# Optimization experiments

Hardware: AMD Instinct MI355X
Metric: run time of the kernel (lower is better)

Reference implementation:

```python
import jax, jax.numpy as jnp
import numpy as np

K = 4
V = 32000
H = 512
B = 16
SOS = 1
EOS = 2


def setup_inputs() -> dict:
    key = jax.random.key(0)
    ks = jax.random.split(key, 8)
    s = 0.08  # small init keeps GRU/log_softmax well-conditioned
    return {
        "enc_h": jax.random.normal(ks[0], (B, H), jnp.float32),
        "E": jax.random.normal(ks[1], (V, H), jnp.float32) * s,
        "W_ih": jax.random.normal(ks[2], (H, 3 * H), jnp.float32) * s,
        "W_hh": jax.random.normal(ks[3], (H, 3 * H), jnp.float32) * s,
        "b_ih": jax.random.normal(ks[4], (3 * H,), jnp.float32) * s,
        "b_hh": jax.random.normal(ks[5], (3 * H,), jnp.float32) * s,
        "Wo": jax.random.normal(ks[6], (H, V), jnp.float32) * s,
        "bo": jax.random.normal(ks[7], (V,), jnp.float32) * s,
        "max_length": 32,
    }


def _beam_search(enc_h, E, W_ih, W_hh, b_ih, b_hh, Wo, bo, T):
    BK = B * K
    pos = jnp.arange(B, dtype=jnp.int32) * K  # pos_index
    # torch .repeat beam inflation: tiled layout (index i -> original i % B)
    h0 = jnp.tile(enc_h, (K, 1))  # [BK, H]
    inp0 = jnp.full((BK,), SOS, dtype=jnp.int32)
    ss0 = jnp.full((BK,), -jnp.inf, dtype=enc_h.dtype).at[pos].set(0.0)

    def gru(x, h):
        gi = x @ W_ih + b_ih
        gh = h @ W_hh + b_hh
        ir, iz, inn = jnp.split(gi, 3, axis=-1)
        hr, hz, hn = jnp.split(gh, 3, axis=-1)
        r = jax.nn.sigmoid(ir + hr)
        z = jax.nn.sigmoid(iz + hz)
        n = jnp.tanh(inn + r * hn)
        return (1.0 - z) * n + z * h

    def fwd_step(carry, _):
        inp, h, ss = carry
        h_new = gru(E[inp], h)                                   # [BK, H]
        logp = jax.nn.log_softmax(h_new @ Wo + bo, axis=-1)      # [BK, V]
        total = (ss[:, None] + logp).reshape(B, K * V)
        scores, cand = jax.lax.top_k(total, K)                   # [B, K]
        symbols = (cand % V).astype(jnp.int32).reshape(-1)       # input_var
        preds = (cand // V + pos[:, None]).astype(jnp.int32).reshape(-1)
        h_sel = h_new[preds]                                     # index_select hidden
        ss_new = scores.reshape(-1)
        ss_masked = jnp.where(symbols == EOS, -jnp.inf, ss_new)  # EOS masking
        return (symbols, h_sel, ss_masked), (logp, ss_new, preds, symbols, h_sel)

    _, (logps, step_scores, preds, syms, hiddens) = jax.lax.scan(
        fwd_step, (inp0, h0, ss0), None, length=T)

    # ---------------- backtrack ----------------
    last = step_scores[-1].reshape(B, K)
    s0, sorted_idx = jax.lax.top_k(last, K)
    tpred0 = (sorted_idx.astype(jnp.int32) + pos[:, None]).reshape(-1)
    lens0 = jnp.full((B, K), T, dtype=jnp.int32)
    hn0 = jnp.zeros((BK, H), dtype=enc_h.dtype)
    eos0 = jnp.zeros((B,), dtype=jnp.int32)

    def bt_step(carry, xs):
        tpred, eosf, s, lens, hn = carry
        logp_t, hid_t, pred_t, sym_t, score_t, tt = xs
        cur_out = logp_t[tpred]
        cur_hid = hid_t[tpred]
        cur_sym = sym_t[tpred]
        new_pred = pred_t[tpred]
        eos = sym_t == EOS
        eos_bk = eos.reshape(B, K).astype(jnp.int32)
        # original loop processes eos hits in descending beam order per batch
        higher = jnp.cumsum(eos_bk[:, ::-1], axis=1)[:, ::-1] - eos_bk
        occ = eosf[:, None] + higher
        res_k = K - occ % K - 1
        res_flat = (pos[:, None] + res_k).reshape(-1)
        idx = jnp.where(eos, res_flat, BK)  # BK = out of bounds -> dropped
        new_pred = new_pred.at[idx].set(pred_t, mode='drop')
        cur_out = cur_out.at[idx].set(logp_t, mode='drop')
        cur_hid = cur_hid.at[idx].set(hid_t, mode='drop')
        hn = hn.at[idx].set(hid_t, mode='drop')
        cur_sym = cur_sym.at[idx].set(sym_t, mode='drop')
        s = s.reshape(-1).at[idx].set(score_t, mode='drop').reshape(B, K)
        lens = lens.reshape(-1).at[idx].set(tt + 1, mode='drop').reshape(B, K)
        eosf = eosf + eos_bk.sum(axis=1)
        return (new_pred, eosf, s, lens, hn), (cur_out, cur_sym)

    ts = jnp.arange(T - 1, -1, -1, dtype=jnp.int32)
    (_, _, s_fin, lens_fin, hn_fin), (outs_rev, syms_rev) = jax.lax.scan(
        bt_step, (tpred0, eos0, s0, lens0, hn0),
        (logps[::-1], hiddens[::-1], preds[::-1], syms[::-1], step_scores[::-1], ts))

    s_sorted, re_idx = jax.lax.top_k(s_fin, K)
    lens_sorted = jnp.take_along_axis(lens_fin, re_idx, axis=1)
    re_flat = (re_idx.astype(jnp.int32) + pos[:, None]).reshape(-1)
    outs = outs_rev[::-1][:, re_flat].reshape(T, B, K, V)
    seqs = syms_rev[::-1][:, re_flat].reshape(T, B, K)
    decoder_outputs = outs[:, :, 0, :]            # [T, B, V]
    decoder_hidden = hn_fin[re_flat].reshape(B, K, H)[:, 0, :]
    return decoder_outputs, decoder_hidden, s_sorted, lens_sorted, seqs


def reference(enc_h, E, W_ih, W_hh, b_ih, b_hh, Wo, bo, max_length):
    return _beam_search(enc_h, E, W_ih, W_hh, b_ih, b_hh, Wo, bo, int(max_length))
```

## Files before the change

kernel.cpp:

```cpp
#include <hip/hip_runtime.h>
#include <math.h>
#include <limits.h>

#define T_STEPS 32
#define BATCH   16
#define KBEAM   4
#define BKR     64
#define HD      512
#define VOC     32000
#define G3      1536
#define SOS_TOK 1
#define EOS_TOK 2
#define NSP     (VOC/64)
#define NE      (NSP*4)
#define NBG     (G3/64)
#define FMBL    2

#define OFF_HCUR   ((size_t)0)
#define OFF_GBUF   (OFF_HCUR + (size_t)BKR*HD)
#define OFF_HNEW   (OFF_GBUF + (size_t)2*BKR*G3)
#define OFF_LSE    (OFF_HNEW + (size_t)T_STEPS*BKR*HD)
#define OFF_SS     (OFF_LSE + (size_t)T_STEPS*BKR)
#define OFF_SCORES (OFF_SS + BKR)
#define OFF_HNFIN  (OFF_SCORES + (size_t)T_STEPS*BKR)
#define OFF_PV     (OFF_HNFIN + (size_t)BKR*HD)
#define OFF_PM     (OFF_PV + (size_t)BKR*NE)
#define OFF_PS     (OFF_PM + (size_t)BKR*NSP)
#define OFF_FEND   (OFF_PS + (size_t)BKR*NSP)
#define IOFF_INP    0
#define IOFF_PREDS  64
#define IOFF_SYMS   (IOFF_PREDS + T_STEPS*BKR)
#define IOFF_RMAP   (IOFF_SYMS + T_STEPS*BKR)
#define IOFF_PC     (IOFF_RMAP + T_STEPS*BATCH)
#define IOFF_GCNT   (IOFF_PC + BKR*NE)
#define IOFF_LCNT   (IOFF_GCNT + T_STEPS)
#define IOFF_END    (IOFF_LCNT + T_STEPS)
#define S_WOH   ((size_t)0)
#define S_WOL   (S_WOH + (size_t)NSP*16*2048)
#define S_WGH   (S_WOL + (size_t)NSP*16*2048)
#define S_WGL   (S_WGH + (size_t)2*NBG*16*2048)
#define S_HNH   (S_WGL + (size_t)2*NBG*16*2048)
#define S_HNL   (S_HNH + (size_t)T_STEPS*BKR*HD)
#define S_HCH   (S_HNL + (size_t)T_STEPS*BKR*HD)
#define S_HCL   (S_HCH + (size_t)BKR*HD)
#define S_EIH   (S_HCL + (size_t)BKR*HD)
#define S_EIL   (S_EIH + (size_t)BKR*HD)
#define S_END   (S_EIL + (size_t)BKR*HD)

#define O_HID  ((size_t)T_STEPS*BATCH*VOC)
#define O_SSRT (O_HID + (size_t)BATCH*HD)
#define O_LENS (O_SSRT + BATCH*KBEAM)
#define O_SEQS (O_LENS + BATCH*KBEAM)

typedef short bf16x8 __attribute__((ext_vector_type(8)));
typedef float f32x4  __attribute__((ext_vector_type(4)));

#define TSZ 2560

__device__ __forceinline__ unsigned short f2bf(float x){
    unsigned u = __float_as_uint(x);
    return (unsigned short)((u + 0x7fffu + ((u >> 16) & 1u)) >> 16);
}
__device__ __forceinline__ float bf2f(unsigned short h){
    return __uint_as_float(((unsigned)h) << 16);
}

__device__ __forceinline__ void dump_C(f32x4 (&acc)[4], float (*Cs)[65], int wave, int lane){
    #pragma unroll
    for (int g = 0; g < 4; ++g){
        int row = g * 16 + (lane >> 4) * 4;
        int col = wave * 16 + (lane & 15);
        #pragma unroll
        for (int r = 0; r < 4; ++r) Cs[row + r][col] = acc[g][r];
    }
}

__device__ __forceinline__ void ins4(float* bv, int* bc, float s, int c){
    bool g0 = (s > bv[0]) || (s == bv[0] && c < bc[0]);
    bool g1 = (s > bv[1]) || (s == bv[1] && c < bc[1]);
    bool g2 = (s > bv[2]) || (s == bv[2] && c < bc[2]);
    bool g3 = (s > bv[3]) || (s == bv[3] && c < bc[3]);
    if (g0){ bv[3]=bv[2];bc[3]=bc[2]; bv[2]=bv[1];bc[2]=bc[1]; bv[1]=bv[0];bc[1]=bc[0]; bv[0]=s; bc[0]=c; }
    else if (g1){ bv[3]=bv[2];bc[3]=bc[2]; bv[2]=bv[1];bc[2]=bc[1]; bv[1]=s; bc[1]=c; }
    else if (g2){ bv[3]=bv[2];bc[3]=bc[2]; bv[2]=s; bc[2]=c; }
    else if (g3){ bv[3]=s; bc[3]=c; }
}


__global__ __launch_bounds__(256) void prepack_kernel(const float* __restrict__ W, int N,
    unsigned short* __restrict__ oh, unsigned short* __restrict__ ol)
{
    const int bx = blockIdx.x, kt = blockIdx.y, tid = threadIdx.x;
    const int bn = tid >> 2, kq = (tid & 3) * 8;
    union { unsigned short u[8]; uint4 v; } h8, l8;
    #pragma unroll
    for (int j = 0; j < 8; ++j){
        float x = W[(size_t)(kt*32 + kq + j) * (size_t)N + bx*64 + bn];
        unsigned short h = f2bf(x);
        h8.u[j] = h; l8.u[j] = f2bf(x - bf2f(h));
    }
    const size_t base = ((size_t)bx*16 + kt) * 2048 + (size_t)tid * 8;
    *(uint4*)(oh + base) = h8.v;
    *(uint4*)(ol + base) = l8.v;
}

__global__ __launch_bounds__(256) void gates_pre_kernel(
    const unsigned short* __restrict__ eih, const unsigned short* __restrict__ eil,
    const unsigned short* __restrict__ hch, const unsigned short* __restrict__ hcl,
    const unsigned short* __restrict__ wgh, const unsigned short* __restrict__ wgl,
    const float* __restrict__ b_ih, const float* __restrict__ b_hh,
    float* __restrict__ gbuf,
    const float* __restrict__ h_cur, float* __restrict__ h_new,
    unsigned short* __restrict__ hnh, unsigned short* __restrict__ hnl,
    int* __restrict__ gcnt)
{
    __shared__ __align__(16) unsigned short sm[2*4*TSZ];
    const int z = blockIdx.y, bx = blockIdx.x, n0 = bx * 64;
    const int tid = threadIdx.x;
    const unsigned short* ahg = z ? hch : eih;
    const unsigned short* alg = z ? hcl : eil;
    const size_t bt = ((size_t)z*NBG + bx) * 16 * 2048;
    const unsigned short* bth = wgh + bt;
    const unsigned short* btl = wgl + bt;
    const int row = tid >> 2, kq = (tid & 3) * 8;
    const int wave = tid >> 6, lane = tid & 63;
    const int fr = lane & 15, fq = lane >> 4;
    const int wr = row * 40 + kq;
    f32x4 acc[4];
    #pragma unroll
    for (int g = 0; g < 4; ++g) acc[g] = (f32x4){0.f,0.f,0.f,0.f};
    {
        uint4 a_h = *(const uint4*)(ahg + (size_t)row*512 + kq);
        uint4 a_l = *(const uint4*)(alg + (size_t)row*512 + kq);
        uint4 b_h = *(const uint4*)(bth + (size_t)tid*8);
        uint4 b_l = *(const uint4*)(btl + (size_t)tid*8);
        *(uint4*)(sm + 0*TSZ + wr) = a_h;
        *(uint4*)(sm + 1*TSZ + wr) = a_l;
        *(uint4*)(sm + 2*TSZ + wr) = b_h;
        *(uint4*)(sm + 3*TSZ + wr) = b_l;
    }
    uint4 pa_h = *(const uint4*)(ahg + (size_t)row*512 + 32 + kq);
    uint4 pa_l = *(const uint4*)(alg + (size_t)row*512 + 32 + kq);
    uint4 pb_h = *(const uint4*)(bth + 2048 + (size_t)tid*8);
    uint4 pb_l = *(const uint4*)(btl + 2048 + (size_t)tid*8);
    __syncthreads();
    #pragma unroll 2
    for (int kt = 0; kt < 16; ++kt){
        unsigned short* cb = sm + (kt & 1) * (4*TSZ);
        unsigned short* nbuf = sm + ((kt & 1) ^ 1) * (4*TSZ);
        uint4 na_h = pa_h, na_l = pa_l, nb_h = pb_h, nb_l = pb_l;
        if (kt < 14){
            na_h = *(const uint4*)(ahg + (size_t)row*512 + (kt+2)*32 + kq);
            na_l = *(const uint4*)(alg + (size_t)row*512 + (kt+2)*32 + kq);
            nb_h = *(const uint4*)(bth + (size_t)(kt+2)*2048 + (size_t)tid*8);
            nb_l = *(const uint4*)(btl + (size_t)(kt+2)*2048 + (size_t)tid*8);
        }
        bf16x8 bh = *(const bf16x8*)(cb + 2*TSZ + (wave*16 + fr)*40 + fq*8);
        bf16x8 bl = *(const bf16x8*)(cb + 3*TSZ + (wave*16 + fr)*40 + fq*8);
        #pragma unroll
        for (int g = 0; g < 4; ++g){
            bf16x8 ah = *(const bf16x8*)(cb + 0*TSZ + (g*16 + fr)*40 + fq*8);
            bf16x8 al = *(const bf16x8*)(cb + 1*TSZ + (g*16 + fr)*40 + fq*8);
            acc[g] = __builtin_amdgcn_mfma_f32_16x16x32_bf16(ah, bh, acc[g], 0, 0, 0);
            acc[g] = __builtin_amdgcn_mfma_f32_16x16x32_bf16(ah, bl, acc[g], 0, 0, 0);
            acc[g] = __builtin_amdgcn_mfma_f32_16x16x32_bf16(al, bh, acc[g], 0, 0, 0);
        }
        if (kt < 15){
            *(uint4*)(nbuf + 0*TSZ + wr) = pa_h;
            *(uint4*)(nbuf + 1*TSZ + wr) = pa_l;
            *(uint4*)(nbuf + 2*TSZ + wr) = pb_h;
            *(uint4*)(nbuf + 3*TSZ + wr) = pb_l;
        }
        __syncthreads();
        pa_h = na_h; pa_l = na_l; pb_h = nb_h; pb_l = nb_l;
    }
    const float* bias = z ? b_hh : b_ih;
    const int col = wave*16 + fr;
    const float bz = bias[n0 + col];
    float* gp = gbuf + (size_t)z * BKR * G3 + n0 + col;
    #pragma unroll
    for (int g = 0; g < 4; ++g){
        const int r0 = g*16 + fq*4;
        #pragma unroll
        for (int r = 0; r < 4; ++r)
            gp[(size_t)(r0 + r) * G3] = acc[g][r] + bz;
    }
    __syncthreads();
    int* comm = (int*)sm;
    if (tid == 0){
        __threadfence();
        comm[0] = atomicAdd(gcnt, 1);
    }
    __syncthreads();
    const int old = comm[0];
    if (old >= 2*NBG - 8 && old < 2*NBG){
        if (tid == 0){
            while (__hip_atomic_load(gcnt, __ATOMIC_ACQUIRE, __HIP_MEMORY_SCOPE_AGENT) < 2*NBG)
                __builtin_amdgcn_s_sleep(1);
        }
        __syncthreads();
        __threadfence();
        const int slice = old - (2*NBG - 8);
        for (int x = tid; x < 64*64; x += 256){
            const int rr = x >> 6, j = (slice << 6) + (x & 63);
            const int xi = rr * HD + j;
            const float* gi = gbuf + (size_t)rr * G3;
            const float* gh = gbuf + (size_t)BKR * G3 + (size_t)rr * G3;
            float ir = gi[j], iz = gi[j + 512], inn = gi[j + 1024];
            float hr = gh[j], hz = gh[j + 512], hnv = gh[j + 1024];
            float r  = 1.f / (1.f + expf(-(ir + hr)));
            float zz = 1.f / (1.f + expf(-(iz + hz)));
            float n  = tanhf(inn + r * hnv);
            float v = (1.f - zz) * n + zz * h_cur[xi];
            h_new[xi] = v;
            unsigned short h = f2bf(v);
            hnh[xi] = h; hnl[xi] = f2bf(v - bf2f(h));
        }
    }
}

__global__ __launch_bounds__(256) void logits_pre_kernel(
    const unsigned short* __restrict__ hnh, const unsigned short* __restrict__ hnl,
    const unsigned short* __restrict__ woh, const unsigned short* __restrict__ wol,
    const float* __restrict__ bo,
    float* __restrict__ pv, int* __restrict__ pc, float* __restrict__ pm, float* __restrict__ ps)
{
    __shared__ __align__(16) unsigned short sm[2*4*TSZ];
    const int bx = blockIdx.x, n0 = bx * 64;
    const int tid = threadIdx.x;
    const unsigned short* bth = woh + (size_t)bx * 16 * 2048;
    const unsigned short* btl = wol + (size_t)bx * 16 * 2048;
    const int row = tid >> 2, kq = (tid & 3) * 8;
    const int wave = tid >> 6, lane = tid & 63;
    const int fr = lane & 15, fq = lane >> 4;
    const int wr = row * 40 + kq;
    f32x4 acc[4];
    #pragma unroll
    for (int g = 0; g < 4; ++g) acc[g] = (f32x4){0.f,0.f,0.f,0.f};
    {
        uint4 a_h = *(const uint4*)(hnh + (size_t)row*512 + kq);
        uint4 a_l = *(const uint4*)(hnl + (size_t)row*512 + kq);
        uint4 b_h = *(const uint4*)(bth + (size_t)tid*8);
        uint4 b_l = *(const uint4*)(btl + (size_t)tid*8);
        *(uint4*)(sm + 0*TSZ + wr) = a_h;
        *(uint4*)(sm + 1*TSZ + wr) = a_l;
        *(uint4*)(sm + 2*TSZ + wr) = b_h;
        *(uint4*)(sm + 3*TSZ + wr) = b_l;
    }
    uint4 pa_h = *(const uint4*)(hnh + (size_t)row*512 + 32 + kq);
    uint4 pa_l = *(const uint4*)(hnl + (size_t)row*512 + 32 + kq);
    uint4 pb_h = *(const uint4*)(bth + 2048 + (size_t)tid*8);
    uint4 pb_l = *(const uint4*)(btl + 2048 + (size_t)tid*8);
    __syncthreads();
    #pragma unroll 2
    for (int kt = 0; kt < 16; ++kt){
        unsigned short* cb = sm + (kt & 1) * (4*TSZ);
        unsigned short* nbuf = sm + ((kt & 1) ^ 1) * (4*TSZ);
        uint4 na_h = pa_h, na_l = pa_l, nb_h = pb_h, nb_l = pb_l;
        if (kt < 14){
            na_h = *(const uint4*)(hnh + (size_t)row*512 + (kt+2)*32 + kq);
            na_l = *(const uint4*)(hnl + (size_t)row*512 + (kt+2)*32 + kq);
            nb_h = *(const uint4*)(bth + (size_t)(kt+2)*2048 + (size_t)tid*8);
            nb_l = *(const uint4*)(btl + (size_t)(kt+2)*2048 + (size_t)tid*8);
        }
        bf16x8 bh = *(const bf16x8*)(cb + 2*TSZ + (wave*16 + fr)*40 + fq*8);
        bf16x8 bl = *(const bf16x8*)(cb + 3*TSZ + (wave*16 + fr)*40 + fq*8);
        #pragma unroll
        for (int g = 0; g < 4; ++g){
            bf16x8 ah = *(const bf16x8*)(cb + 0*TSZ + (g*16 + fr)*40 + fq*8);
            bf16x8 al = *(const bf16x8*)(cb + 1*TSZ + (g*16 + fr)*40 + fq*8);
            acc[g] = __builtin_amdgcn_mfma_f32_16x16x32_bf16(ah, bh, acc[g], 0, 0, 0);
            acc[g] = __builtin_amdgcn_mfma_f32_16x16x32_bf16(ah, bl, acc[g], 0, 0, 0);
            acc[g] = __builtin_amdgcn_mfma_f32_16x16x32_bf16(al, bh, acc[g], 0, 0, 0);
        }
        if (kt < 15){
            *(uint4*)(nbuf + 0*TSZ + wr) = pa_h;
            *(uint4*)(nbuf + 1*TSZ + wr) = pa_l;
            *(uint4*)(nbuf + 2*TSZ + wr) = pb_h;
            *(uint4*)(nbuf + 3*TSZ + wr) = pb_l;
        }
        __syncthreads();
        pa_h = na_h; pa_l = na_l; pb_h = nb_h; pb_l = nb_l;
    }
    float (*Cs)[65] = (float(*)[65])sm;
    dump_C(acc, Cs, wave, lane);
    __syncthreads();
    const int c0 = (tid & 3) * 16;
    float bv[4] = {-INFINITY,-INFINITY,-INFINITY,-INFINITY};
    int bc[4] = {INT_MAX, INT_MAX, INT_MAX, INT_MAX};
    float m = -INFINITY, s = 0.f;
    #pragma unroll
    for (int j = 0; j < 16; ++j){
        float x = Cs[row][c0 + j] + bo[n0 + c0 + j];
        if (x > m){ s = s * expf(m - x) + 1.f; m = x; }
        else s += expf(x - m);
        ins4(bv, bc, x, n0 + c0 + j);
    }
    #pragma unroll
    for (int o = 1; o < 4; o <<= 1){
        float ov[4]; int oc[4];
        #pragma unroll
        for (int q = 0; q < 4; ++q){ ov[q] = __shfl_xor(bv[q], o); oc[q] = __shfl_xor(bc[q], o); }
        #pragma unroll
        for (int q = 0; q < 4; ++q) ins4(bv, bc, ov[q], oc[q]);
        float m2 = __shfl_xor(m, o), s2 = __shfl_xor(s, o);
        float M = fmaxf(m, m2);
        s = s * expf(m - M) + s2 * expf(m2 - M);
        m = M;
    }
    if ((tid & 3) == 0){
        const size_t base = (size_t)row * NE + (size_t)bx * 4;
        #pragma unroll
        for (int q = 0; q < 4; ++q){ pv[base + q] = bv[q]; pc[base + q] = bc[q]; }
        pm[row * NSP + bx] = m; ps[row * NSP + bx] = s;
    }
}

__global__ __launch_bounds__(256) void final_pre_kernel(
    const unsigned short* __restrict__ hnh, const unsigned short* __restrict__ hnl,
    const int* __restrict__ rmap, const float* __restrict__ lse_all,
    const unsigned short* __restrict__ woh, const unsigned short* __restrict__ wol,
    const float* __restrict__ bo, float* __restrict__ out)
{
    __shared__ __align__(16) unsigned short sm[2*6*TSZ];
    __shared__ int sidx[64*FMBL]; __shared__ float subm[64*FMBL];
    const int tid = threadIdx.x;
    const int bx = blockIdx.y, n0 = bx * 64;
    const int mbase = blockIdx.x * (64 * FMBL);
    if (tid < 64*FMBL){ int g = rmap[mbase + tid]; sidx[tid] = g; subm[tid] = lse_all[g]; }
    __syncthreads();
    const int row = tid >> 2, kq = (tid & 3) * 8;
    const int wave = tid >> 6, lane = tid & 63;
    const int fr = lane & 15, fq = lane >> 4;
    const int wr = row * 40 + kq;
    const size_t r0 = (size_t)sidx[row] * 512;
    const size_t r1 = (size_t)sidx[64 + row] * 512;
    const unsigned short* bth = woh + (size_t)bx * 16 * 2048;
    const unsigned short* btl = wol + (size_t)bx * 16 * 2048;
    f32x4 acc[FMBL][4];
    #pragma unroll
    for (int mb = 0; mb < FMBL; ++mb)
        #pragma unroll
        for (int g = 0; g < 4; ++g) acc[mb][g] = (f32x4){0.f,0.f,0.f,0.f};
    {
        uint4 a0h = *(const uint4*)(hnh + r0 + kq);
        uint4 a0l = *(const uint4*)(hnl + r0 + kq);
        uint4 a1h = *(const uint4*)(hnh + r1 + kq);
        uint4 a1l = *(const uint4*)(hnl + r1 + kq);
        uint4 b_h = *(const uint4*)(bth + (size_t)tid*8);
        uint4 b_l = *(const uint4*)(btl + (size_t)tid*8);
        *(uint4*)(sm + 0*TSZ + wr) = a0h;
        *(uint4*)(sm + 1*TSZ + wr) = a0l;
        *(uint4*)(sm + 2*TSZ + wr) = a1h;
        *(uint4*)(sm + 3*TSZ + wr) = a1l;
        *(uint4*)(sm + 4*TSZ + wr) = b_h;
        *(uint4*)(sm + 5*TSZ + wr) = b_l;
    }
    uint4 p0h = *(const uint4*)(hnh + r0 + 32 + kq);
    uint4 p0l = *(const uint4*)(hnl + r0 + 32 + kq);
    uint4 p1h = *(const uint4*)(hnh + r1 + 32 + kq);
    uint4 p1l = *(const uint4*)(hnl + r1 + 32 + kq);
    uint4 pbh = *(const uint4*)(bth + 2048 + (size_t)tid*8);
    uint4 pbl = *(const uint4*)(btl + 2048 + (size_t)tid*8);
    __syncthreads();
    #pragma unroll 2
    for (int kt = 0; kt < 16; ++kt){
        unsigned short* cb = sm + (kt & 1) * (6*TSZ);
        unsigned short* nbuf = sm + ((kt & 1) ^ 1) * (6*TSZ);
        uint4 n0h = p0h, n0l = p0l, n1h = p1h, n1l = p1l, nbh = pbh, nbl = pbl;
        if (kt < 14){
            n0h = *(const uint4*)(hnh + r0 + (kt+2)*32 + kq);
            n0l = *(const uint4*)(hnl + r0 + (kt+2)*32 + kq);
            n1h = *(const uint4*)(hnh + r1 + (kt+2)*32 + kq);
            n1l = *(const uint4*)(hnl + r1 + (kt+2)*32 + kq);
            nbh = *(const uint4*)(bth + (size_t)(kt+2)*2048 + (size_t)tid*8);
            nbl = *(const uint4*)(btl + (size_t)(kt+2)*2048 + (size_t)tid*8);
        }
        bf16x8 bh = *(const bf16x8*)(cb + 4*TSZ + (wave*16 + fr)*40 + fq*8);
        bf16x8 bl = *(const bf16x8*)(cb + 5*TSZ + (wave*16 + fr)*40 + fq*8);
        #pragma unroll
        for (int mb = 0; mb < FMBL; ++mb){
            #pragma unroll
            for (int g = 0; g < 4; ++g){
                bf16x8 ah = *(const bf16x8*)(cb + (2*mb+0)*TSZ + (g*16 + fr)*40 + fq*8);
                bf16x8 al = *(const bf16x8*)(cb + (2*mb+1)*TSZ + (g*16 + fr)*40 + fq*8);
                acc[mb][g] = __builtin_amdgcn_mfma_f32_16x16x32_bf16(ah, bh, acc[mb][g], 0, 0, 0);
                acc[mb][g] = __builtin_amdgcn_mfma_f32_16x16x32_bf16(ah, bl, acc[mb][g], 0, 0, 0);
                acc[mb][g] = __builtin_amdgcn_mfma_f32_16x16x32_bf16(al, bh, acc[mb][g], 0, 0, 0);
            }
        }
        if (kt < 15){
            *(uint4*)(nbuf + 0*TSZ + wr) = p0h;
            *(uint4*)(nbuf + 1*TSZ + wr) = p0l;
            *(uint4*)(nbuf + 2*TSZ + wr) = p1h;
            *(uint4*)(nbuf + 3*TSZ + wr) = p1l;
            *(uint4*)(nbuf + 4*TSZ + wr) = pbh;
            *(uint4*)(nbuf + 5*TSZ + wr) = pbl;
        }
        __syncthreads();
        p0h = n0h; p0l = n0l; p1h = n1h; p1l = n1l; pbh = nbh; pbl = nbl;
    }
    const int col = n0 + wave*16 + fr;
    const float bz = bo[col];
    #pragma unroll
    for (int mb = 0; mb < FMBL; ++mb){
        #pragma unroll
        for (int g = 0; g < 4; ++g){
            const int rb = mb*64 + g*16 + fq*4;
            #pragma unroll
            for (int r = 0; r < 4; ++r){
                const int rowi = rb + r;
                out[(size_t)(mbase + rowi) * VOC + col] = acc[mb][g][r] + bz - subm[rowi];
            }
        }
    }
}

__device__ __forceinline__ void mfma_core(
    const float* __restrict__ Abase, const int* __restrict__ ridx, int mbase,
    const float* __restrict__ B, int ldb, int n0,
    unsigned short (&Ah)[64][40], unsigned short (&Al)[64][40],
    unsigned short (&Bh)[64][40], unsigned short (&Bl)[64][40],
    int (&sidx)[64], f32x4 (&acc)[4])
{
    const int tid = threadIdx.x;
    if (tid < 64) sidx[tid] = ridx ? ridx[mbase + tid] : (mbase + tid);
    #pragma unroll
    for (int g = 0; g < 4; ++g) acc[g] = (f32x4){0.f, 0.f, 0.f, 0.f};
    const int wave = tid >> 6, lane = tid & 63;
    const int am = tid >> 2, ak0 = (tid & 3) * 8;
    const int bn = tid & 63, br0 = (tid >> 6) * 8;
    __syncthreads();
    const float* bcol = B + n0 + bn;
    for (int kt = 0; kt < 16; ++kt){
        {
            const float* ap = Abase + (size_t)sidx[am] * HD + kt * 32 + ak0;
            float4 x0 = *(const float4*)ap, x1 = *(const float4*)(ap + 4);
            float xs[8] = {x0.x, x0.y, x0.z, x0.w, x1.x, x1.y, x1.z, x1.w};
            union { unsigned short u[8]; uint4 v; } h8, l8;
            #pragma unroll
            for (int j = 0; j < 8; ++j){
                unsigned short h = f2bf(xs[j]);
                h8.u[j] = h; l8.u[j] = f2bf(xs[j] - bf2f(h));
            }
            *(uint4*)&Ah[am][ak0] = h8.v;
            *(uint4*)&Al[am][ak0] = l8.v;
        }
        {
            const float* bp = bcol + (size_t)(kt * 32 + br0) * ldb;
            union { unsigned short u[8]; uint4 v; } h8, l8;
            #pragma unroll
            for (int j = 0; j < 8; ++j){
                float x = bp[(size_t)j * ldb];
                unsigned short h = f2bf(x);
                h8.u[j] = h; l8.u[j] = f2bf(x - bf2f(h));
            }
            *(uint4*)&Bh[bn][br0] = h8.v;
            *(uint4*)&Bl[bn][br0] = l8.v;
        }
        __syncthreads();
        bf16x8 bh = *(const bf16x8*)&Bh[wave * 16 + (lane & 15)][(lane >> 4) * 8];
        bf16x8 bl = *(const bf16x8*)&Bl[wave * 16 + (lane & 15)][(lane >> 4) * 8];
        #pragma unroll
        for (int g = 0; g < 4; ++g){
            bf16x8 ah = *(const bf16x8*)&Ah[g * 16 + (lane & 15)][(lane >> 4) * 8];
            bf16x8 al = *(const bf16x8*)&Al[g * 16 + (lane & 15)][(lane >> 4) * 8];
            acc[g] = __builtin_amdgcn_mfma_f32_16x16x32_bf16(ah, bh, acc[g], 0, 0, 0);
            acc[g] = __builtin_amdgcn_mfma_f32_16x16x32_bf16(ah, bl, acc[g], 0, 0, 0);
            acc[g] = __builtin_amdgcn_mfma_f32_16x16x32_bf16(al, bh, acc[g], 0, 0, 0);
        }
        __syncthreads();
    }
}

__global__ __launch_bounds__(256) void gates_mfma_kernel(
    const float* __restrict__ E, const int* __restrict__ inp, const float* __restrict__ h_cur,
    const float* __restrict__ W_ih, const float* __restrict__ W_hh,
    const float* __restrict__ b_ih, const float* __restrict__ b_hh,
    float* __restrict__ gbuf)
{
    __shared__ unsigned short Ah[64][40], Al[64][40], Bh[64][40], Bl[64][40];
    __shared__ int sidx[64];
    __shared__ float Cs[64][65];
    const int z = blockIdx.y;
    const int n0 = blockIdx.x * 64;
    const int tid = threadIdx.x;
    f32x4 acc[4];
    mfma_core(z ? h_cur : E, z ? nullptr : inp, 0,
              z ? W_hh : W_ih, G3, n0, Ah, Al, Bh, Bl, sidx, acc);
    dump_C(acc, Cs, tid >> 6, tid & 63);
    __syncthreads();
    const float* bias = z ? b_hh : b_ih;
    const int row = tid >> 2, c0 = (tid & 3) * 16;
    float* gp = gbuf + (size_t)z * BKR * G3 + (size_t)row * G3 + n0 + c0;
    #pragma unroll
    for (int q = 0; q < 4; ++q){
        float4 bz = *(const float4*)(bias + n0 + c0 + q * 4);
        float4 v;
        v.x = Cs[row][c0 + q*4 + 0] + bz.x;
        v.y = Cs[row][c0 + q*4 + 1] + bz.y;
        v.z = Cs[row][c0 + q*4 + 2] + bz.z;
        v.w = Cs[row][c0 + q*4 + 3] + bz.w;
        *(float4*)(gp + q * 4) = v;
    }
}

__global__ __launch_bounds__(256) void logits_topk_kernel(const float* __restrict__ h_new,
    const float* __restrict__ Wo, const float* __restrict__ bo,
    float* __restrict__ pv, int* __restrict__ pc, float* __restrict__ pm, float* __restrict__ ps)
{
    __shared__ unsigned short Ah[64][40], Al[64][40], Bh[64][40], Bl[64][40];
    __shared__ int sidx[64];
    __shared__ float Cs[64][65];
    const int bx = blockIdx.x, n0 = bx * 64;
    const int tid = threadIdx.x;
    f32x4 acc[4];
    mfma_core(h_new, nullptr, 0, Wo, VOC, n0, Ah, Al, Bh, Bl, sidx, acc);
    dump_C(acc, Cs, tid >> 6, tid & 63);
    __syncthreads();
    const int row = tid >> 2, c0 = (tid & 3) * 16;
    float bv[4] = {-INFINITY,-INFINITY,-INFINITY,-INFINITY};
    int bc[4] = {INT_MAX, INT_MAX, INT_MAX, INT_MAX};
    float m = -INFINITY, s = 0.f;
    #pragma unroll
    for (int j = 0; j < 16; ++j){
        float x = Cs[row][c0 + j] + bo[n0 + c0 + j];
        if (x > m){ s = s * expf(m - x) + 1.f; m = x; }
        else s += expf(x - m);
        ins4(bv, bc, x, n0 + c0 + j);
    }
    #pragma unroll
    for (int o = 1; o < 4; o <<= 1){
        float ov[4]; int oc[4];
        #pragma unroll
        for (int q = 0; q < 4; ++q){ ov[q] = __shfl_xor(bv[q], o); oc[q] = __shfl_xor(bc[q], o); }
        #pragma unroll
        for (int q = 0; q < 4; ++q) ins4(bv, bc, ov[q], oc[q]);
        float m2 = __shfl_xor(m, o), s2 = __shfl_xor(s, o);
        float M = fmaxf(m, m2);
        s = s * expf(m - M) + s2 * expf(m2 - M);
        m = M;
    }
    if ((tid & 3) == 0){
        const size_t base = (size_t)row * NE + (size_t)bx * 4;
        #pragma unroll
        for (int q = 0; q < 4; ++q){ pv[base + q] = bv[q]; pc[base + q] = bc[q]; }
        pm[row * NSP + bx] = m; ps[row * NSP + bx] = s;
    }
}

__global__ __launch_bounds__(256) void final_mfma_kernel(const float* __restrict__ h_new_all,
    const int* __restrict__ rmap, const float* __restrict__ lse_all,
    const float* __restrict__ Wo, const float* __restrict__ bo, float* __restrict__ out)
{
    __shared__ unsigned short Ah[64][40], Al[64][40], Bh[64][40], Bl[64][40];
    __shared__ int sidx[64];
    __shared__ float Cs[64][65];
    __shared__ float subm[64];
    const int n0 = blockIdx.x * 64, mb = blockIdx.y * 64;
    const int tid = threadIdx.x;
    f32x4 acc[4];
    mfma_core(h_new_all, rmap, mb, Wo, VOC, n0, Ah, Al, Bh, Bl, sidx, acc);
    dump_C(acc, Cs, tid >> 6, tid & 63);
    if (tid < 64) subm[tid] = lse_all[sidx[tid]];
    __syncthreads();
    const int row = tid >> 2, c0 = (tid & 3) * 16;
    const float sub = subm[row];
    float* op = out + (size_t)(mb + row) * VOC + n0 + c0;
    #pragma unroll
    for (int q = 0; q < 4; ++q){
        float4 bz = *(const float4*)(bo + n0 + c0 + q * 4);
        float4 v;
        v.x = Cs[row][c0 + q*4 + 0] + bz.x - sub;
        v.y = Cs[row][c0 + q*4 + 1] + bz.y - sub;
        v.z = Cs[row][c0 + q*4 + 2] + bz.z - sub;
        v.w = Cs[row][c0 + q*4 + 3] + bz.w - sub;
        *(float4*)(op + q * 4) = v;
    }
}


__global__ void gru_combine_kernel(const float* __restrict__ gbuf, const float* __restrict__ h_cur,
    float* __restrict__ h_new, unsigned short* __restrict__ hnh, unsigned short* __restrict__ hnl)
{
    int x = blockIdx.x * 256 + threadIdx.x;
    int i = x >> 9, j = x & 511;
    const float* gi = gbuf + (size_t)i * G3;
    const float* gh = gbuf + (size_t)BKR * G3 + (size_t)i * G3;
    float ir = gi[j], iz = gi[j + 512], inn = gi[j + 1024];
    float hr = gh[j], hz = gh[j + 512], hnv = gh[j + 1024];
    float r  = 1.f / (1.f + expf(-(ir + hr)));
    float zz = 1.f / (1.f + expf(-(iz + hz)));
    float n  = tanhf(inn + r * hnv);
    float v = (1.f - zz) * n + zz * h_cur[x];
    h_new[x] = v;
    if (hnh){
        unsigned short h = f2bf(v);
        hnh[x] = h; hnl[x] = f2bf(v - bf2f(h));
    }
}

__global__ __launch_bounds__(256) void topk_phase_b(
    const float* __restrict__ pv, const int* __restrict__ pc,
    const float* __restrict__ pm, const float* __restrict__ ps,
    int t,
    float* __restrict__ scores_all, int* __restrict__ preds_all, int* __restrict__ syms_all,
    float* __restrict__ ss, int* __restrict__ inp, float* __restrict__ lse_all,
    const float* __restrict__ h_new, float* __restrict__ h_cur,
    const float* __restrict__ E,
    unsigned short* __restrict__ hch, unsigned short* __restrict__ hcl,
    unsigned short* __restrict__ eih, unsigned short* __restrict__ eil)
{
    const int b = blockIdx.x, tid = threadIdx.x;
    const int wave = tid >> 6, lane = tid & 63;
    const int row = b * KBEAM + wave;

    float bv[4] = {-INFINITY,-INFINITY,-INFINITY,-INFINITY};
    int bc[4] = {INT_MAX, INT_MAX, INT_MAX, INT_MAX};
    for (int e = lane; e < NE; e += 64)
        ins4(bv, bc, pv[(size_t)row * NE + e], pc[(size_t)row * NE + e]);
    #pragma unroll
    for (int o = 1; o < 64; o <<= 1){
        float ov[4]; int oc[4];
        #pragma unroll
        for (int q = 0; q < 4; ++q){ ov[q] = __shfl_xor(bv[q], o); oc[q] = __shfl_xor(bc[q], o); }
        #pragma unroll
        for (int q = 0; q < 4; ++q) ins4(bv, bc, ov[q], oc[q]);
    }
    float m = -INFINITY, s = 0.f;
    for (int e = lane; e < NSP; e += 64){
        float m2 = pm[row * NSP + e], s2 = ps[row * NSP + e];
        float M = fmaxf(m, m2);
        s = s * expf(m - M) + s2 * expf(m2 - M);
        m = M;
    }
    #pragma unroll
    for (int o = 1; o < 64; o <<= 1){
        float m2 = __shfl_xor(m, o), s2 = __shfl_xor(s, o);
        float M = fmaxf(m, m2);
        s = s * expf(m - M) + s2 * expf(m2 - M);
        m = M;
    }
    __shared__ float rtv[KBEAM][4]; __shared__ int rtc[KBEAM][4];
    __shared__ float rlse[KBEAM];
    if (lane == 0){
        #pragma unroll
        for (int q = 0; q < 4; ++q){ rtv[wave][q] = bv[q]; rtc[wave][q] = bc[q]; }
        rlse[wave] = m + logf(s);
    }
    __syncthreads();
    __shared__ int spred[KBEAM]; __shared__ int ssym[KBEAM];
    if (tid == 0){
        float gv[4] = {-INFINITY,-INFINITY,-INFINITY,-INFINITY};
        int gc[4] = {INT_MAX, INT_MAX, INT_MAX, INT_MAX};
        #pragma unroll
        for (int kl = 0; kl < KBEAM; ++kl){
            const int r2 = b * KBEAM + kl;
            float lse = rlse[kl];
            lse_all[t * BKR + r2] = lse;
            float off = ss[r2] - lse;
            if (off == -INFINITY){
                #pragma unroll
                for (int q = 0; q < 4; ++q) ins4(gv, gc, -INFINITY, kl * VOC + q);
            } else {
                #pragma unroll
                for (int q = 0; q < 4; ++q) ins4(gv, gc, rtv[kl][q] + off, kl * VOC + rtc[kl][q]);
            }
        }
        #pragma unroll
        for (int u = 0; u < KBEAM; ++u){
            int cand = gc[u]; float val = gv[u];
            int sym = cand % VOC; int pg = b * KBEAM + cand / VOC;
            int slot = b * KBEAM + u;
            scores_all[t * BKR + slot] = val;
            syms_all[t * BKR + slot] = sym;
            preds_all[t * BKR + slot] = pg;
            ss[slot] = (sym == EOS_TOK) ? -INFINITY : val;
            inp[slot] = sym;
            spred[u] = pg; ssym[u] = sym;
        }
    }
    __syncthreads();
    for (int x = tid; x < KBEAM * HD; x += 256){
        int u = x >> 9, j = x & 511;
        const int idx = (b * KBEAM + u) * HD + j;
        float v = h_new[spred[u] * HD + j];
        h_cur[idx] = v;
        if (hch){
            unsigned short h = f2bf(v);
            hch[idx] = h; hcl[idx] = f2bf(v - bf2f(h));
            float e = E[(size_t)ssym[u] * HD + j];
            unsigned short eh = f2bf(e);
            eih[idx] = eh; eil[idx] = f2bf(e - bf2f(eh));
        }
    }
}

__global__ void init_kernel(const float* __restrict__ enc_h, const float* __restrict__ E,
    float* __restrict__ h_cur, float* __restrict__ ss, int* __restrict__ inp,
    unsigned short* __restrict__ hch, unsigned short* __restrict__ hcl,
    unsigned short* __restrict__ eih, unsigned short* __restrict__ eil,
    int* __restrict__ cnts)
{
    const int i = blockIdx.x;
    for (int j = threadIdx.x; j < HD; j += blockDim.x){
        float v = enc_h[(i & (BATCH - 1)) * HD + j];
        h_cur[i * HD + j] = v;
        if (hch){
            const int idx = i * HD + j;
            unsigned short h = f2bf(v);
            hch[idx] = h; hcl[idx] = f2bf(v - bf2f(h));
            float e = E[(size_t)SOS_TOK * HD + j];
            unsigned short eh = f2bf(e);
            eih[idx] = eh; eil[idx] = f2bf(e - bf2f(eh));
        }
    }
    if (i == 0 && threadIdx.x < BKR){
        ss[threadIdx.x] = ((threadIdx.x & (KBEAM - 1)) == 0) ? 0.f : -INFINITY;
        inp[threadIdx.x] = SOS_TOK;
    }
    if (i == 1 && cnts){
        for (int x = threadIdx.x; x < 2*T_STEPS; x += blockDim.x) cnts[x] = 0;
    }
}

__global__ __launch_bounds__(256) void backtrack_kernel(
    const float* __restrict__ scores_all, const int* __restrict__ preds_all, const int* __restrict__ syms_all,
    const float* __restrict__ h_new_all, float* __restrict__ hn_fin,
    int* __restrict__ rmap, float* __restrict__ out)
{
    __shared__ int   l_syms[T_STEPS*BKR];
    __shared__ int   l_preds[T_STEPS*BKR];
    __shared__ float l_scores[T_STEPS*BKR];
    __shared__ int   outrow_s[T_STEPS*BKR];
    __shared__ int   cursym_s[T_STEPS*BKR];
    __shared__ int tpred[64]; __shared__ float sfin[64]; __shared__ int lensq[64];
    __shared__ int eosf[BATCH];
    __shared__ int orow[64], csym[64], npred_s[64];
    __shared__ int cp_slot[64], cp_src[64]; __shared__ int nc_b[BATCH];
    __shared__ int reidx[64];
    const int tid = threadIdx.x;

    for (int x = tid; x < T_STEPS*BKR; x += 256){
        l_syms[x]   = syms_all[x];
        l_preds[x]  = preds_all[x];
        l_scores[x] = scores_all[x];
    }
    for (int x = tid; x < BKR*HD; x += 256) hn_fin[x] = 0.f;
    __syncthreads();

    if (tid < BATCH){
        const int b = tid;
        float v[KBEAM]; int used[KBEAM];
        #pragma unroll
        for (int k = 0; k < KBEAM; ++k){ v[k] = l_scores[(T_STEPS-1)*BKR + b*KBEAM + k]; used[k] = 0; }
        #pragma unroll
        for (int u = 0; u < KBEAM; ++u){
            int best = -1; float bvv = 0.f;
            #pragma unroll
            for (int k = 0; k < KBEAM; ++k) if (!used[k] && (best < 0 || v[k] > bvv)){ best = k; bvv = v[k]; }
            used[best] = 1;
            tpred[b*KBEAM+u] = b*KBEAM + best;
            sfin[b*KBEAM+u] = bvv;
            lensq[b*KBEAM+u] = T_STEPS;
        }
        eosf[b] = 0;
    }
    __syncthreads();

    for (int t = T_STEPS-1; t >= 0; --t){
        if (tid < 64){
            int tp = tpred[tid];
            orow[tid]    = tp;
            csym[tid]    = l_syms[t*BKR + tp];
            npred_s[tid] = l_preds[t*BKR + tp];
        }
        __syncthreads();
        if (tid < BATCH){
            const int b = tid;
            int eos[KBEAM]; int cnt = 0;
            #pragma unroll
            for (int k = 0; k < KBEAM; ++k) eos[k] = (l_syms[t*BKR + b*KBEAM + k] == EOS_TOK);
            int nc = 0;
            #pragma unroll
            for (int k = 0; k < KBEAM; ++k) if (eos[k]){
                int higher = 0;
                #pragma unroll
                for (int k2 = k+1; k2 < KBEAM; ++k2) higher += eos[k2];
                int occ = eosf[b] + higher;
                int rk = KBEAM - (occ % KBEAM) - 1;
                int slot = b*KBEAM + rk;
                int j = b*KBEAM + k;
                npred_s[slot] = l_preds[t*BKR + j];
                orow[slot]    = j;
                csym[slot]    = l_syms[t*BKR + j];
                sfin[slot]    = l_scores[t*BKR + j];
                lensq[slot]   = t + 1;
                cp_slot[b*KBEAM + nc] = slot;
                cp_src[b*KBEAM + nc]  = l_preds[t*BKR + j];
                ++nc; ++cnt;
            }
            nc_b[b] = nc;
            eosf[b] += cnt;
        }
        __syncthreads();
        if (tid < 64){
            outrow_s[t*BKR + tid] = orow[tid];
            cursym_s[t*BKR + tid] = csym[tid];
            tpred[tid] = npred_s[tid];
        }
        {
            const int e = tid >> 2;
            const int eb = e >> 2, eq = e & 3;
            if (eq < nc_b[eb]){
                const int slot = cp_slot[eb*KBEAM + eq];
                const int src  = cp_src[eb*KBEAM + eq];
                const float4* sp = (const float4*)(h_new_all + (size_t)(t*BKR + src)*HD);
                float4* dp = (float4*)(hn_fin + (size_t)slot*HD);
                for (int j = (tid & 3); j < HD/4; j += 4) dp[j] = sp[j];
            }
        }
        __syncthreads();
    }

    if (tid < BATCH){
        const int b = tid;
        float v[KBEAM]; int used[KBEAM];
        #pragma unroll
        for (int k = 0; k < KBEAM; ++k){ v[k] = sfin[b*KBEAM+k]; used[k] = 0; }
        #pragma unroll
        for (int u = 0; u < KBEAM; ++u){
            int best = -1; float bvv = 0.f;
            #pragma unroll
            for (int k = 0; k < KBEAM; ++k) if (!used[k] && (best < 0 || v[k] > bvv)){ best = k; bvv = v[k]; }
            used[best] = 1;
            reidx[b*KBEAM+u] = best;
            out[O_SSRT + b*KBEAM + u] = bvv;
            out[O_LENS + b*KBEAM + u] = (float)lensq[b*KBEAM + best];
        }
    }
    __syncthreads();
    for (int x = tid; x < T_STEPS*BATCH; x += 256){
        int t2 = x >> 4, b = x & 15;
        rmap[x] = t2*BKR + outrow_s[t2*BKR + b*KBEAM + reidx[b*KBEAM]];
    }
    for (int x = tid; x < T_STEPS*BKR; x += 256){
        int t2 = x >> 6, rem = x & 63, b = rem >> 2, k = rem & 3;
        out[O_SEQS + x] = (float)cursym_s[t2*BKR + b*KBEAM + reidx[b*KBEAM + k]];
    }
    for (int x = tid; x < BATCH*HD; x += 256){
        int b = x >> 9, j = x & 511;
        out[O_HID + x] = hn_fin[(b*KBEAM + reidx[b*KBEAM])*HD + j];
    }
}

extern "C" void kernel_launch(void* const* d_in, const int* in_sizes, int n_in,
                              void* d_out, int out_size, void* d_ws, size_t ws_size,
                              hipStream_t stream)
{
    const float* enc_h = (const float*)d_in[0];
    const float* E     = (const float*)d_in[1];
    const float* W_ih  = (const float*)d_in[2];
    const float* W_hh  = (const float*)d_in[3];
    const float* b_ih  = (const float*)d_in[4];
    const float* b_hh  = (const float*)d_in[5];
    const float* Wo    = (const float*)d_in[6];
    const float* bo    = (const float*)d_in[7];
    float* out = (float*)d_out;

    float* w = (float*)d_ws;
    float* h_cur      = w + OFF_HCUR;
    float* gbuf       = w + OFF_GBUF;
    float* h_new_all  = w + OFF_HNEW;
    float* lse_all    = w + OFF_LSE;
    float* ss         = w + OFF_SS;
    float* scores_all = w + OFF_SCORES;
    float* hn_fin     = w + OFF_HNFIN;
    float* pv         = w + OFF_PV;
    float* pm         = w + OFF_PM;
    float* ps         = w + OFF_PS;
    int* wi         = (int*)(w + OFF_FEND);
    int* inp        = wi + IOFF_INP;
    int* preds_all  = wi + IOFF_PREDS;
    int* syms_all   = wi + IOFF_SYMS;
    int* rmap       = wi + IOFF_RMAP;
    int* pc         = wi + IOFF_PC;
    int* gcnt       = wi + IOFF_GCNT;
    unsigned short* sb = (unsigned short*)(wi + IOFF_END);
    unsigned short* woh = sb + S_WOH;
    unsigned short* wol = sb + S_WOL;
    unsigned short* wgh = sb + S_WGH;
    unsigned short* wgl = sb + S_WGL;
    unsigned short* hnh = sb + S_HNH;
    unsigned short* hnl = sb + S_HNL;
    unsigned short* hch = sb + S_HCH;
    unsigned short* hcl = sb + S_HCL;
    unsigned short* eih = sb + S_EIH;
    unsigned short* eil = sb + S_EIL;

    const size_t NEED = (size_t)OFF_FEND*4 + (size_t)IOFF_END*4 + (size_t)S_END*2;
    const bool pre = (ws_size >= NEED);

    init_kernel<<<dim3(BKR), 256, 0, stream>>>(enc_h, E, h_cur, ss, inp,
        pre ? hch : nullptr, hcl, eih, eil, pre ? gcnt : nullptr);
    if (pre){
        prepack_kernel<<<dim3(NSP, 16), 256, 0, stream>>>(Wo, VOC, woh, wol);
        prepack_kernel<<<dim3(NBG, 16), 256, 0, stream>>>(W_ih, G3, wgh, wgl);
        prepack_kernel<<<dim3(NBG, 16), 256, 0, stream>>>(W_hh, G3,
            wgh + (size_t)NBG*16*2048, wgl + (size_t)NBG*16*2048);
    }
    for (int t = 0; t < T_STEPS; ++t){
        float* h_new_t = h_new_all + (size_t)t * BKR * HD;
        unsigned short* hnh_t = hnh + (size_t)t * BKR * HD;
        unsigned short* hnl_t = hnl + (size_t)t * BKR * HD;
        if (pre){
            gates_pre_kernel<<<dim3(NBG, 2), 256, 0, stream>>>(eih, eil, hch, hcl,
                wgh, wgl, b_ih, b_hh, gbuf, h_cur, h_new_t, hnh_t, hnl_t, gcnt + t);
            logits_pre_kernel<<<dim3(NSP), 256, 0, stream>>>(hnh_t, hnl_t, woh, wol, bo,
                pv, pc, pm, ps);
            topk_phase_b<<<dim3(BATCH), 256, 0, stream>>>(pv, pc, pm, ps, t, scores_all, preds_all, syms_all,
                ss, inp, lse_all, h_new_t, h_cur, E,
                hch, hcl, eih, eil);
        } else {
            gates_mfma_kernel<<<dim3(NBG, 2), 256, 0, stream>>>(E, inp, h_cur, W_ih, W_hh, b_ih, b_hh, gbuf);
            gru_combine_kernel<<<dim3(BKR*HD/256), 256, 0, stream>>>(gbuf, h_cur, h_new_t,
                nullptr, hnl_t);
            logits_topk_kernel<<<dim3(NSP), 256, 0, stream>>>(h_new_t, Wo, bo, pv, pc, pm, ps);
            topk_phase_b<<<dim3(BATCH), 256, 0, stream>>>(pv, pc, pm, ps, t, scores_all, preds_all, syms_all,
                ss, inp, lse_all, h_new_t, h_cur, E,
                nullptr, hcl, eih, eil);
        }
    }
    backtrack_kernel<<<dim3(1), 256, 0, stream>>>(scores_all, preds_all, syms_all, h_new_all, hn_fin,
                                                  rmap, out);
    if (pre){
        final_pre_kernel<<<dim3((T_STEPS*BATCH)/(64*FMBL), NSP), 256, 0, stream>>>(
            hnh, hnl, rmap, lse_all, woh, wol, bo, out);
    } else {
        final_mfma_kernel<<<dim3(NSP, T_STEPS*BATCH/64), 256, 0, stream>>>(h_new_all, rmap, lse_all, Wo, bo, out);
    }
}
```

Measured before the change: 3.023 ms.

## Drop LDS staging in MFMA GEMM kernels and load fragments directly from global

Removes the double-buffered shared-memory staging of A and B tiles in the gates, logits and final-output GEMM kernels. Each wave now loads its MFMA fragments straight from global memory, with the A fragments of the gathered-row kernel taken through precomputed row indices. This drops the LDS writes, the per-k-tile barriers and the LDS footprint, which may allow more blocks per CU. In exchange, A fragments are loaded redundantly by all four waves and the loads are less coalesced, relying on L1/L2 to absorb the duplication, and there is no explicit prefetch pipelining.

After: 4.277 ms. +41.5%, slower.

```diff
diff --git a/kernel.cpp b/kernel.cpp
--- a/kernel.cpp
+++ b/kernel.cpp
@@ -55,8 +55,6 @@
 typedef short bf16x8 __attribute__((ext_vector_type(8)));
 typedef float f32x4  __attribute__((ext_vector_type(4)));
 
-#define TSZ 2560
-
 __device__ __forceinline__ unsigned short f2bf(float x){
     unsigned u = __float_as_uint(x);
     return (unsigned short)((u + 0x7fffu + ((u >> 16) & 1u)) >> 16);
@@ -114,65 +112,33 @@
     unsigned short* __restrict__ hnh, unsigned short* __restrict__ hnl,
     int* __restrict__ gcnt)
 {
-    __shared__ __align__(16) unsigned short sm[2*4*TSZ];
+    __shared__ int comm[1];
     const int z = blockIdx.y, bx = blockIdx.x, n0 = bx * 64;
     const int tid = threadIdx.x;
     const unsigned short* ahg = z ? hch : eih;
     const unsigned short* alg = z ? hcl : eil;
     const size_t bt = ((size_t)z*NBG + bx) * 16 * 2048;
-    const unsigned short* bth = wgh + bt;
-    const unsigned short* btl = wgl + bt;
-    const int row = tid >> 2, kq = (tid & 3) * 8;
     const int wave = tid >> 6, lane = tid & 63;
     const int fr = lane & 15, fq = lane >> 4;
-    const int wr = row * 40 + kq;
+    const unsigned short* bh_p = wgh + bt + (wave*16 + fr)*32 + fq*8;
+    const unsigned short* bl_p = wgl + bt + (wave*16 + fr)*32 + fq*8;
+    const unsigned short* ah_p = ahg + (size_t)fr*512 + fq*8;
+    const unsigned short* al_p = alg + (size_t)fr*512 + fq*8;
     f32x4 acc[4];
     #pragma unroll
     for (int g = 0; g < 4; ++g) acc[g] = (f32x4){0.f,0.f,0.f,0.f};
-    {
-        uint4 a_h = *(const uint4*)(ahg + (size_t)row*512 + kq);
-        uint4 a_l = *(const uint4*)(alg + (size_t)row*512 + kq);
-        uint4 b_h = *(const uint4*)(bth + (size_t)tid*8);
-        uint4 b_l = *(const uint4*)(btl + (size_t)tid*8);
-        *(uint4*)(sm + 0*TSZ + wr) = a_h;
-        *(uint4*)(sm + 1*TSZ + wr) = a_l;
-        *(uint4*)(sm + 2*TSZ + wr) = b_h;
-        *(uint4*)(sm + 3*TSZ + wr) = b_l;
-    }
-    uint4 pa_h = *(const uint4*)(ahg + (size_t)row*512 + 32 + kq);
-    uint4 pa_l = *(const uint4*)(alg + (size_t)row*512 + 32 + kq);
-    uint4 pb_h = *(const uint4*)(bth + 2048 + (size_t)tid*8);
-    uint4 pb_l = *(const uint4*)(btl + 2048 + (size_t)tid*8);
-    __syncthreads();
-    #pragma unroll 2
+    #pragma unroll 4
     for (int kt = 0; kt < 16; ++kt){
-        unsigned short* cb = sm + (kt & 1) * (4*TSZ);
-        unsigned short* nbuf = sm + ((kt & 1) ^ 1) * (4*TSZ);
-        uint4 na_h = pa_h, na_l = pa_l, nb_h = pb_h, nb_l = pb_l;
-        if (kt < 14){
-            na_h = *(const uint4*)(ahg + (size_t)row*512 + (kt+2)*32 + kq);
-            na_l = *(const uint4*)(alg + (size_t)row*512 + (kt+2)*32 + kq);
-            nb_h = *(const uint4*)(bth + (size_t)(kt+2)*2048 + (size_t)tid*8);
-            nb_l = *(const uint4*)(btl + (size_t)(kt+2)*2048 + (size_t)tid*8);
-        }
-        bf16x8 bh = *(const bf16x8*)(cb + 2*TSZ + (wave*16 + fr)*40 + fq*8);
-        bf16x8 bl = *(const bf16x8*)(cb + 3*TSZ + (wave*16 + fr)*40 + fq*8);
+        bf16x8 bh = *(const bf16x8*)(bh_p + kt*2048);
+        bf16x8 bl = *(const bf16x8*)(bl_p + kt*2048);
         #pragma unroll
         for (int g = 0; g < 4; ++g){
-            bf16x8 ah = *(const bf16x8*)(cb + 0*TSZ + (g*16 + fr)*40 + fq*8);
-            bf16x8 al = *(const bf16x8*)(cb + 1*TSZ + (g*16 + fr)*40 + fq*8);
+            bf16x8 ah = *(const bf16x8*)(ah_p + g*16*512 + kt*32);
+            bf16x8 al = *(const bf16x8*)(al_p + g*16*512 + kt*32);
             acc[g] = __builtin_amdgcn_mfma_f32_16x16x32_bf16(ah, bh, acc[g], 0, 0, 0);
             acc[g] = __builtin_amdgcn_mfma_f32_16x16x32_bf16(ah, bl, acc[g], 0, 0, 0);
             acc[g] = __builtin_amdgcn_mfma_f32_16x16x32_bf16(al, bh, acc[g], 0, 0, 0);
         }
-        if (kt < 15){
-            *(uint4*)(nbuf + 0*TSZ + wr) = pa_h;
-            *(uint4*)(nbuf + 1*TSZ + wr) = pa_l;
-            *(uint4*)(nbuf + 2*TSZ + wr) = pb_h;
-            *(uint4*)(nbuf + 3*TSZ + wr) = pb_l;
-        }
-        __syncthreads();
-        pa_h = na_h; pa_l = na_l; pb_h = nb_h; pb_l = nb_l;
     }
     const float* bias = z ? b_hh : b_ih;
     const int col = wave*16 + fr;
@@ -186,7 +152,6 @@
             gp[(size_t)(r0 + r) * G3] = acc[g][r] + bz;
     }
     __syncthreads();
-    int* comm = (int*)sm;
     if (tid == 0){
         __threadfence();
         comm[0] = atomicAdd(gcnt, 1);
@@ -225,67 +190,34 @@
     const float* __restrict__ bo,
     float* __restrict__ pv, int* __restrict__ pc, float* __restrict__ pm, float* __restrict__ ps)
 {
-    __shared__ __align__(16) unsigned short sm[2*4*TSZ];
+    __shared__ float Cs[64][65];
     const int bx = blockIdx.x, n0 = bx * 64;
     const int tid = threadIdx.x;
-    const unsigned short* bth = woh + (size_t)bx * 16 * 2048;
-    const unsigned short* btl = wol + (size_t)bx * 16 * 2048;
-    const int row = tid >> 2, kq = (tid & 3) * 8;
     const int wave = tid >> 6, lane = tid & 63;
     const int fr = lane & 15, fq = lane >> 4;
-    const int wr = row * 40 + kq;
+    const unsigned short* bh_p = woh + (size_t)bx*16*2048 + (wave*16 + fr)*32 + fq*8;
+    const unsigned short* bl_p = wol + (size_t)bx*16*2048 + (wave*16 + fr)*32 + fq*8;
+    const unsigned short* ah_p = hnh + (size_t)fr*512 + fq*8;
+    const unsigned short* al_p = hnl + (size_t)fr*512 + fq*8;
     f32x4 acc[4];
     #pragma unroll
     for (int g = 0; g < 4; ++g) acc[g] = (f32x4){0.f,0.f,0.f,0.f};
-    {
-        uint4 a_h = *(const uint4*)(hnh + (size_t)row*512 + kq);
-        uint4 a_l = *(const uint4*)(hnl + (size_t)row*512 + kq);
-        uint4 b_h = *(const uint4*)(bth + (size_t)tid*8);
-        uint4 b_l = *(const uint4*)(btl + (size_t)tid*8);
-        *(uint4*)(sm + 0*TSZ + wr) = a_h;
-        *(uint4*)(sm + 1*TSZ + wr) = a_l;
-        *(uint4*)(sm + 2*TSZ + wr) = b_h;
-        *(uint4*)(sm + 3*TSZ + wr) = b_l;
-    }
-    uint4 pa_h = *(const uint4*)(hnh + (size_t)row*512 + 32 + kq);
-    uint4 pa_l = *(const uint4*)(hnl + (size_t)row*512 + 32 + kq);
-    uint4 pb_h = *(const uint4*)(bth + 2048 + (size_t)tid*8);
-    uint4 pb_l = *(const uint4*)(btl + 2048 + (size_t)tid*8);
-    __syncthreads();
-    #pragma unroll 2
+    #pragma unroll 4
     for (int kt = 0; kt < 16; ++kt){
-        unsigned short* cb = sm + (kt & 1) * (4*TSZ);
-        unsigned short* nbuf = sm + ((kt & 1) ^ 1) * (4*TSZ);
-        uint4 na_h = pa_h, na_l = pa_l, nb_h = pb_h, nb_l = pb_l;
-        if (kt < 14){
-            na_h = *(const uint4*)(hnh + (size_t)row*512 + (kt+2)*32 + kq);
-            na_l = *(const uint4*)(hnl + (size_t)row*512 + (kt+2)*32 + kq);
-            nb_h = *(const uint4*)(bth + (size_t)(kt+2)*2048 + (size_t)tid*8);
-            nb_l = *(const uint4*)(btl + (size_t)(kt+2)*2048 + (size_t)tid*8);
-        }
-        bf16x8 bh = *(const bf16x8*)(cb + 2*TSZ + (wave*16 + fr)*40 + fq*8);
-        bf16x8 bl = *(const bf16x8*)(cb + 3*TSZ + (wave*16 + fr)*40 + fq*8);
+        bf16x8 bh = *(const bf16x8*)(bh_p + kt*2048);
+        bf16x8 bl = *(const bf16x8*)(bl_p + kt*2048);
         #pragma unroll
         for (int g = 0; g < 4; ++g){
-            bf16x8 ah = *(const bf16x8*)(cb + 0*TSZ + (g*16 + fr)*40 + fq*8);
-            bf16x8 al = *(const bf16x8*)(cb + 1*TSZ + (g*16 + fr)*40 + fq*8);
+            bf16x8 ah = *(const bf16x8*)(ah_p + g*16*512 + kt*32);
+            bf16x8 al = *(const bf16x8*)(al_p + g*16*512 + kt*32);
             acc[g] = __builtin_amdgcn_mfma_f32_16x16x32_bf16(ah, bh, acc[g], 0, 0, 0);
             acc[g] = __builtin_amdgcn_mfma_f32_16x16x32_bf16(ah, bl, acc[g], 0, 0, 0);
             acc[g] = __builtin_amdgcn_mfma_f32_16x16x32_bf16(al, bh, acc[g], 0, 0, 0);
         }
-        if (kt < 15){
-            *(uint4*)(nbuf + 0*TSZ + wr) = pa_h;
-            *(uint4*)(nbuf + 1*TSZ + wr) = pa_l;
-            *(uint4*)(nbuf + 2*TSZ + wr) = pb_h;
-            *(uint4*)(nbuf + 3*TSZ + wr) = pb_l;
-        }
-        __syncthreads();
-        pa_h = na_h; pa_l = na_l; pb_h = nb_h; pb_l = nb_l;
-    }
-    float (*Cs)[65] = (float(*)[65])sm;
+    }
     dump_C(acc, Cs, wave, lane);
     __syncthreads();
-    const int c0 = (tid & 3) * 16;
+    const int row = tid >> 2, c0 = (tid & 3) * 16;
     float bv[4] = {-INFINITY,-INFINITY,-INFINITY,-INFINITY};
     int bc[4] = {INT_MAX, INT_MAX, INT_MAX, INT_MAX};
     float m = -INFINITY, s = 0.f;
@@ -322,83 +254,42 @@
     const unsigned short* __restrict__ woh, const unsigned short* __restrict__ wol,
     const float* __restrict__ bo, float* __restrict__ out)
 {
-    __shared__ __align__(16) unsigned short sm[2*6*TSZ];
     __shared__ int sidx[64*FMBL]; __shared__ float subm[64*FMBL];
     const int tid = threadIdx.x;
     const int bx = blockIdx.y, n0 = bx * 64;
     const int mbase = blockIdx.x * (64 * FMBL);
     if (tid < 64*FMBL){ int g = rmap[mbase + tid]; sidx[tid] = g; subm[tid] = lse_all[g]; }
     __syncthreads();
-    const int row = tid >> 2, kq = (tid & 3) * 8;
     const int wave = tid >> 6, lane = tid & 63;
     const int fr = lane & 15, fq = lane >> 4;
-    const int wr = row * 40 + kq;
-    const size_t r0 = (size_t)sidx[row] * 512;
-    const size_t r1 = (size_t)sidx[64 + row] * 512;
-    const unsigned short* bth = woh + (size_t)bx * 16 * 2048;
-    const unsigned short* btl = wol + (size_t)bx * 16 * 2048;
+    int rows[FMBL*4];
+    #pragma unroll
+    for (int mb = 0; mb < FMBL; ++mb)
+        #pragma unroll
+        for (int g = 0; g < 4; ++g) rows[mb*4 + g] = sidx[mb*64 + g*16 + fr];
+    const unsigned short* bh_p = woh + (size_t)bx*16*2048 + (wave*16 + fr)*32 + fq*8;
+    const unsigned short* bl_p = wol + (size_t)bx*16*2048 + (wave*16 + fr)*32 + fq*8;
     f32x4 acc[FMBL][4];
     #pragma unroll
     for (int mb = 0; mb < FMBL; ++mb)
         #pragma unroll
         for (int g = 0; g < 4; ++g) acc[mb][g] = (f32x4){0.f,0.f,0.f,0.f};
-    {
-        uint4 a0h = *(const uint4*)(hnh + r0 + kq);
-        uint4 a0l = *(const uint4*)(hnl + r0 + kq);
-        uint4 a1h = *(const uint4*)(hnh + r1 + kq);
-        uint4 a1l = *(const uint4*)(hnl + r1 + kq);
-        uint4 b_h = *(const uint4*)(bth + (size_t)tid*8);
-        uint4 b_l = *(const uint4*)(btl + (size_t)tid*8);
-        *(uint4*)(sm + 0*TSZ + wr) = a0h;
-        *(uint4*)(sm + 1*TSZ + wr) = a0l;
-        *(uint4*)(sm + 2*TSZ + wr) = a1h;
-        *(uint4*)(sm + 3*TSZ + wr) = a1l;
-        *(uint4*)(sm + 4*TSZ + wr) = b_h;
-        *(uint4*)(sm + 5*TSZ + wr) = b_l;
-    }
-    uint4 p0h = *(const uint4*)(hnh + r0 + 32 + kq);
-    uint4 p0l = *(const uint4*)(hnl + r0 + 32 + kq);
-    uint4 p1h = *(const uint4*)(hnh + r1 + 32 + kq);
-    uint4 p1l = *(const uint4*)(hnl + r1 + 32 + kq);
-    uint4 pbh = *(const uint4*)(bth + 2048 + (size_t)tid*8);
-    uint4 pbl = *(const uint4*)(btl + 2048 + (size_t)tid*8);
-    __syncthreads();
     #pragma unroll 2
     for (int kt = 0; kt < 16; ++kt){
-        unsigned short* cb = sm + (kt & 1) * (6*TSZ);
-        unsigned short* nbuf = sm + ((kt & 1) ^ 1) * (6*TSZ);
-        uint4 n0h = p0h, n0l = p0l, n1h = p1h, n1l = p1l, nbh = pbh, nbl = pbl;
-        if (kt < 14){
-            n0h = *(const uint4*)(hnh + r0 + (kt+2)*32 + kq);
-            n0l = *(const uint4*)(hnl + r0 + (kt+2)*32 + kq);
-            n1h = *(const uint4*)(hnh + r1 + (kt+2)*32 + kq);
-            n1l = *(const uint4*)(hnl + r1 + (kt+2)*32 + kq);
-            nbh = *(const uint4*)(bth + (size_t)(kt+2)*2048 + (size_t)tid*8);
-            nbl = *(const uint4*)(btl + (size_t)(kt+2)*2048 + (size_t)tid*8);
-        }
-        bf16x8 bh = *(const bf16x8*)(cb + 4*TSZ + (wave*16 + fr)*40 + fq*8);
-        bf16x8 bl = *(const bf16x8*)(cb + 5*TSZ + (wave*16 + fr)*40 + fq*8);
+        bf16x8 bh = *(const bf16x8*)(bh_p + kt*2048);
+        bf16x8 bl = *(const bf16x8*)(bl_p + kt*2048);
         #pragma unroll
         for (int mb = 0; mb < FMBL; ++mb){
             #pragma unroll
             for (int g = 0; g < 4; ++g){
-                bf16x8 ah = *(const bf16x8*)(cb + (2*mb+0)*TSZ + (g*16 + fr)*40 + fq*8);
-                bf16x8 al = *(const bf16x8*)(cb + (2*mb+1)*TSZ + (g*16 + fr)*40 + fq*8);
+                const size_t ao = (size_t)rows[mb*4 + g] * 512 + kt*32 + fq*8;
+                bf16x8 ah = *(const bf16x8*)(hnh + ao);
+                bf16x8 al = *(const bf16x8*)(hnl + ao);
                 acc[mb][g] = __builtin_amdgcn_mfma_f32_16x16x32_bf16(ah, bh, acc[mb][g], 0, 0, 0);
                 acc[mb][g] = __builtin_amdgcn_mfma_f32_16x16x32_bf16(ah, bl, acc[mb][g], 0, 0, 0);
                 acc[mb][g] = __builtin_amdgcn_mfma_f32_16x16x32_bf16(al, bh, acc[mb][g], 0, 0, 0);
             }
         }
-        if (kt < 15){
-            *(uint4*)(nbuf + 0*TSZ + wr) = p0h;
-            *(uint4*)(nbuf + 1*TSZ + wr) = p0l;
-            *(uint4*)(nbuf + 2*TSZ + wr) = p1h;
-            *(uint4*)(nbuf + 3*TSZ + wr) = p1l;
-            *(uint4*)(nbuf + 4*TSZ + wr) = pbh;
-            *(uint4*)(nbuf + 5*TSZ + wr) = pbl;
-        }
-        __syncthreads();
-        p0h = n0h; p0l = n0l; p1h = n1h; p1l = n1l; pbh = nbh; pbl = nbl;
     }
     const int col = n0 + wave*16 + fr;
     const float bz = bo[col];
```
